# Kernel tuning notes

Hardware: AMD Instinct MI355X
Metric: run time of the kernel (lower is better)

## Reference

```python
import jax, jax.numpy as jnp
import numpy as np

LN_EPS = 1e-12


def setup_inputs() -> dict:
    key = jax.random.key(0)
    ks = jax.random.split(key, 6)
    B, S, H = 32, 512, 768
    P, K = 76, 64
    V, E = 50257, 768
    return {
        "sequence_data": jax.random.normal(ks[0], (B, S, H), dtype=jnp.float32),
        "masked_positions": jax.random.randint(ks[1], (B, P), 0, S, dtype=jnp.int64),
        "candidate_sets": jax.random.randint(ks[2], (B, P, K), 0, V, dtype=jnp.int64),
        "embedding_table": jax.random.normal(ks[3], (V, E), dtype=jnp.float32) * 0.02,
        "dense_w": jax.random.normal(ks[4], (H, E), dtype=jnp.float32) * (1.0 / np.sqrt(H)),
        "dense_b": jnp.zeros((E,), dtype=jnp.float32),
        "ln_gamma": jnp.ones((E,), dtype=jnp.float32),
        "ln_beta": jnp.zeros((E,), dtype=jnp.float32),
    }


def reference(sequence_data, masked_positions, candidate_sets, embedding_table,
              dense_w, dense_b, ln_gamma, ln_beta):
    # Gather masked positions: [B, P, H]
    gathered = jnp.take_along_axis(
        sequence_data, masked_positions[:, :, None], axis=1)
    # Dense (no activation), then LayerNorm (eps=1e-12)
    lm = jnp.einsum('bph,he->bpe', gathered, dense_w) + dense_b
    mu = jnp.mean(lm, axis=-1, keepdims=True)
    var = jnp.mean(jnp.square(lm - mu), axis=-1, keepdims=True)
    lm = (lm - mu) * jax.lax.rsqrt(var + LN_EPS) * ln_gamma + ln_beta
    # Candidate embedding gather: [B, P, K, E]
    cand = embedding_table[candidate_sets]
    # Inner products -> logits [B, P, K]
    logits = jnp.einsum('bpe,bpke->bpk', lm, cand)
    return logits
```

## Files before the change

### kernel.cpp

```cpp
#include <hip/hip_runtime.h>

typedef __attribute__((ext_vector_type(8))) short bf16x8;
typedef __attribute__((ext_vector_type(4))) float f32x4;

#define HH 768
#define EE 768
#define BB 32
#define SS 512
#define PP 76
#define KCAND 64
#define MM (BB * PP)
#define VV 50257
#define NC (MM * KCAND)
#define CAP 16
#define OVF_CAP 4096

#define OFF_WT    0u
#define OFF_AG    1179648u
#define OFF_LM    4915200u
#define OFF_LMN   12386304u
#define OFF_CUR   16121856u
#define OFF_PERM2 16322896u
#define OFF_OVF   19539344u

#define WT_BLOCKS 576
#define AG_BLOCKS 304
#define ZR_BLOCKS 197
#define GEMM_BLOCKS 456
#define SC_BLOCKS 608
#define ROW_BLOCKS 12565
#define OVF_BLOCKS 32

__device__ inline unsigned short f2bf(float f) {
    unsigned int u = __float_as_uint(f);
    u += 0x7fffu + ((u >> 16) & 1u);
    return (unsigned short)(u >> 16);
}
__device__ inline float bf2f(unsigned short h) {
    return __uint_as_float(((unsigned int)h) << 16);
}

__global__ __launch_bounds__(256) void prep_kernel(
    const float* __restrict__ W, unsigned short* __restrict__ Wt,
    const float* __restrict__ seq, const int* __restrict__ mpos,
    unsigned short* __restrict__ Ag, int* __restrict__ cursor) {
    const int bid = blockIdx.x;
    if (bid < WT_BLOCKS) {
        __shared__ float tile[32][33];
        const int h0 = (bid % 24) * 32, e0 = (bid / 24) * 32;
        const int c = threadIdx.x & 31, r = threadIdx.x >> 5;
#pragma unroll
        for (int rr = r; rr < 32; rr += 8)
            tile[rr][c] = W[(size_t)(h0 + rr) * EE + e0 + c];
        __syncthreads();
#pragma unroll
        for (int rr = r; rr < 32; rr += 8)
            Wt[(size_t)(e0 + rr) * HH + h0 + c] = f2bf(tile[c][rr]);
    } else if (bid < WT_BLOCKS + AG_BLOCKS) {
        const int m0 = (bid - WT_BLOCKS) * 8;
        const int t = threadIdx.x;
#pragma unroll
        for (int rr = 0; rr < 8; ++rr) {
            const int m = m0 + rr;
            const int b = m / PP, p = m - b * PP;
            const int ps = mpos[b * PP + p];
            const float* srow = seq + (size_t)(b * SS + ps) * HH;
            unsigned short* drow = Ag + (size_t)m * HH;
#pragma unroll
            for (int j = 0; j < 3; ++j)
                drow[t + j * 256] = f2bf(srow[t + j * 256]);
        }
    } else {
        const int i = (bid - WT_BLOCKS - AG_BLOCKS) * 256 + threadIdx.x;
        if (i <= VV) cursor[i] = 0;
    }
}

__global__ __launch_bounds__(256) void gemm_scatter_kernel(
    const unsigned short* __restrict__ Ag, const unsigned short* __restrict__ Wt,
    float* __restrict__ lm, const int* __restrict__ cand,
    int* __restrict__ cursor, int* __restrict__ perm2, int* __restrict__ ovf) {
    const int bid = blockIdx.x;
    if (bid < GEMM_BLOCKS) {
        __shared__ unsigned short Alds[64][72];
        __shared__ unsigned short Blds[64][72];
        const int bn = bid % 12, bm = bid / 12;
        const int tid = threadIdx.x;
        const int sr = tid >> 2, sc = (tid & 3) * 16;
        const unsigned short* abase = Ag + (size_t)(bm * 64) * HH;
        const unsigned short* bbase = Wt + (size_t)(bn * 64) * HH;
        const int lane = tid & 63, wv = tid >> 6;
        const int wm = wv >> 1, wn = wv & 1;
        const int fr = lane & 15, fq = (lane >> 4) * 8;
        f32x4 acc[2][2] = {};
        for (int kk = 0; kk < HH; kk += 64) {
            __syncthreads();
            *(int4*)&Alds[sr][sc]     = *(const int4*)(abase + (size_t)sr * HH + kk + sc);
            *(int4*)&Alds[sr][sc + 8] = *(const int4*)(abase + (size_t)sr * HH + kk + sc + 8);
            *(int4*)&Blds[sr][sc]     = *(const int4*)(bbase + (size_t)sr * HH + kk + sc);
            *(int4*)&Blds[sr][sc + 8] = *(const int4*)(bbase + (size_t)sr * HH + kk + sc + 8);
            __syncthreads();
#pragma unroll
            for (int ks = 0; ks < 64; ks += 32) {
                bf16x8 af[2], bfr[2];
#pragma unroll
                for (int t = 0; t < 2; ++t)
                    af[t] = *(const bf16x8*)&Alds[wm * 32 + t * 16 + fr][ks + fq];
#pragma unroll
                for (int t = 0; t < 2; ++t)
                    bfr[t] = *(const bf16x8*)&Blds[wn * 32 + t * 16 + fr][ks + fq];
#pragma unroll
                for (int tm = 0; tm < 2; ++tm)
#pragma unroll
                    for (int tn = 0; tn < 2; ++tn)
                        acc[tm][tn] = __builtin_amdgcn_mfma_f32_16x16x32_bf16(
                            af[tm], bfr[tn], acc[tm][tn], 0, 0, 0);
            }
        }
#pragma unroll
        for (int tm = 0; tm < 2; ++tm)
#pragma unroll
            for (int tn = 0; tn < 2; ++tn) {
                const int col = bn * 64 + wn * 32 + tn * 16 + (lane & 15);
                const int rbase = bm * 64 + wm * 32 + tm * 16 + (lane >> 4) * 4;
#pragma unroll
                for (int g = 0; g < 4; ++g)
                    lm[(size_t)(rbase + g) * EE + col] = acc[tm][tn][g];
            }
    } else {
        const int i = (bid - GEMM_BLOCKS) * 256 + threadIdx.x;
        const int row = cand[i];
        const int slot = atomicAdd(&cursor[row], 1);
        if (slot < CAP) {
            perm2[row * CAP + slot] = i;
        } else {
            const int j = atomicAdd(&cursor[VV], 1);
            if (j < OVF_CAP) ovf[j] = i;
        }
    }
}

__global__ __launch_bounds__(256) void ln_kernel(
    const float* __restrict__ lm, const float* __restrict__ bias,
    const float* __restrict__ gamma, const float* __restrict__ beta,
    unsigned short* __restrict__ lmn) {
    const int lane = threadIdx.x & 63;
    const int m = blockIdx.x * 4 + (threadIdx.x >> 6);
    const float4* x4 = (const float4*)(lm + (size_t)m * EE);
    const float4* b4 = (const float4*)bias;
    const float4* g4 = (const float4*)gamma;
    const float4* e4 = (const float4*)beta;
    float x[12], g[12], e[12];
    {
        const float4 X0 = x4[lane * 2], X1 = x4[lane * 2 + 1], X2 = x4[128 + lane];
        const float4 B0 = b4[lane * 2], B1 = b4[lane * 2 + 1], B2 = b4[128 + lane];
        const float4 G0 = g4[lane * 2], G1 = g4[lane * 2 + 1], G2 = g4[128 + lane];
        const float4 E0 = e4[lane * 2], E1 = e4[lane * 2 + 1], E2 = e4[128 + lane];
        x[0]=X0.x+B0.x; x[1]=X0.y+B0.y; x[2]=X0.z+B0.z; x[3]=X0.w+B0.w;
        x[4]=X1.x+B1.x; x[5]=X1.y+B1.y; x[6]=X1.z+B1.z; x[7]=X1.w+B1.w;
        x[8]=X2.x+B2.x; x[9]=X2.y+B2.y; x[10]=X2.z+B2.z; x[11]=X2.w+B2.w;
        g[0]=G0.x; g[1]=G0.y; g[2]=G0.z; g[3]=G0.w;
        g[4]=G1.x; g[5]=G1.y; g[6]=G1.z; g[7]=G1.w;
        g[8]=G2.x; g[9]=G2.y; g[10]=G2.z; g[11]=G2.w;
        e[0]=E0.x; e[1]=E0.y; e[2]=E0.z; e[3]=E0.w;
        e[4]=E1.x; e[5]=E1.y; e[6]=E1.z; e[7]=E1.w;
        e[8]=E2.x; e[9]=E2.y; e[10]=E2.z; e[11]=E2.w;
    }
    float s = 0.f, q = 0.f;
#pragma unroll
    for (int i = 0; i < 12; ++i) { s += x[i]; q += x[i] * x[i]; }
#pragma unroll
    for (int m2 = 32; m2; m2 >>= 1) { s += __shfl_xor(s, m2); q += __shfl_xor(q, m2); }
    const float mu = s * (1.0f / 768.0f);
    const float rstd = rsqrtf(q * (1.0f / 768.0f) - mu * mu + 1e-12f);
    unsigned short o8[8];
#pragma unroll
    for (int i = 0; i < 8; ++i) o8[i] = f2bf((x[i] - mu) * rstd * g[i] + e[i]);
    *(int4*)(lmn + (size_t)m * EE + lane * 8) = *(const int4*)o8;
    unsigned short o4[4];
#pragma unroll
    for (int i = 0; i < 4; ++i) o4[i] = f2bf((x[8 + i] - mu) * rstd * g[8 + i] + e[8 + i]);
    *(ushort2*)(lmn + (size_t)m * EE + 512 + lane * 4) = *(const ushort2*)o4;
    *(ushort2*)(lmn + (size_t)m * EE + 512 + lane * 4 + 2) = *(const ushort2*)(o4 + 2);
}

__global__ __launch_bounds__(256) void group_logits_kernel(
    const float* __restrict__ emb, const unsigned short* __restrict__ lmn,
    const int* __restrict__ cursor, const int* __restrict__ perm2,
    const int* __restrict__ ovf, const int* __restrict__ cand,
    float* __restrict__ out) {
    const int lane = threadIdx.x & 63;
    const int bid = blockIdx.x;
    if (bid < ROW_BLOCKS) {
        const int r = bid * 4 + (threadIdx.x >> 6);
        if (r >= VV) return;
        int c = cursor[r];
        if (c == 0) return;
        if (c > CAP) c = CAP;
        const float4* e4 = (const float4*)(emb + (size_t)r * EE);
        const float4 E0 = e4[lane * 2], E1 = e4[lane * 2 + 1], E2 = e4[128 + lane];
        const int l8 = lane * 8, l4 = 512 + lane * 4;
        const int base = r * CAP;
        for (int o = 0; o < c; o += 4) {
            const int nn = c - o;
            int idxv[4]; bf16x8 c8[4]; ushort4 c4v[4];
#pragma unroll
            for (int j = 0; j < 4; ++j) {
                const int jj = (j < nn) ? j : 0;
                const int idx = perm2[base + o + jj];
                idxv[j] = idx;
                const unsigned short* lrow = lmn + (size_t)(idx >> 6) * EE;
                c8[j] = *(const bf16x8*)(lrow + l8);
                c4v[j] = *(const ushort4*)(lrow + l4);
            }
            float d[4];
#pragma unroll
            for (int j = 0; j < 4; ++j) {
                d[j] = bf2f((unsigned short)c8[j][0]) * E0.x
                     + bf2f((unsigned short)c8[j][1]) * E0.y
                     + bf2f((unsigned short)c8[j][2]) * E0.z
                     + bf2f((unsigned short)c8[j][3]) * E0.w
                     + bf2f((unsigned short)c8[j][4]) * E1.x
                     + bf2f((unsigned short)c8[j][5]) * E1.y
                     + bf2f((unsigned short)c8[j][6]) * E1.z
                     + bf2f((unsigned short)c8[j][7]) * E1.w
                     + bf2f(c4v[j].x) * E2.x + bf2f(c4v[j].y) * E2.y
                     + bf2f(c4v[j].z) * E2.z + bf2f(c4v[j].w) * E2.w;
            }
#pragma unroll
            for (int m2 = 32; m2; m2 >>= 1) {
#pragma unroll
                for (int j = 0; j < 4; ++j) d[j] += __shfl_xor(d[j], m2);
            }
            if (lane == 0) {
#pragma unroll
                for (int j = 0; j < 4; ++j)
                    if (j < nn) out[idxv[j]] = d[j];
            }
        }
    } else {
        const int nov0 = cursor[VV];
        const int nov = nov0 < OVF_CAP ? nov0 : OVF_CAP;
        const int wid = (bid - ROW_BLOCKS) * 4 + (threadIdx.x >> 6);
        const int l8 = lane * 8, l4 = 512 + lane * 4;
        for (int j = wid; j < nov; j += OVF_BLOCKS * 4) {
            const int idx = ovf[j];
            const int r = cand[idx];
            const float4* e4 = (const float4*)(emb + (size_t)r * EE);
            const float4 E0 = e4[lane * 2], E1 = e4[lane * 2 + 1], E2 = e4[128 + lane];
            const unsigned short* lrow = lmn + (size_t)(idx >> 6) * EE;
            const bf16x8 c8 = *(const bf16x8*)(lrow + l8);
            const ushort4 c4v = *(const ushort4*)(lrow + l4);
            float d = bf2f((unsigned short)c8[0]) * E0.x + bf2f((unsigned short)c8[1]) * E0.y
                    + bf2f((unsigned short)c8[2]) * E0.z + bf2f((unsigned short)c8[3]) * E0.w
                    + bf2f((unsigned short)c8[4]) * E1.x + bf2f((unsigned short)c8[5]) * E1.y
                    + bf2f((unsigned short)c8[6]) * E1.z + bf2f((unsigned short)c8[7]) * E1.w
                    + bf2f(c4v.x) * E2.x + bf2f(c4v.y) * E2.y
                    + bf2f(c4v.z) * E2.z + bf2f(c4v.w) * E2.w;
#pragma unroll
            for (int m2 = 32; m2; m2 >>= 1) d += __shfl_xor(d, m2);
            if (lane == 0) out[idx] = d;
        }
    }
}

extern "C" void kernel_launch(void* const* d_in, const int* in_sizes, int n_in,
                              void* d_out, int out_size, void* d_ws, size_t ws_size,
                              hipStream_t stream) {
    const float* seq   = (const float*)d_in[0];
    const int*   mpos  = (const int*)d_in[1];
    const int*   cand  = (const int*)d_in[2];
    const float* emb   = (const float*)d_in[3];
    const float* W     = (const float*)d_in[4];
    const float* bias  = (const float*)d_in[5];
    const float* gamma = (const float*)d_in[6];
    const float* beta  = (const float*)d_in[7];
    float* out = (float*)d_out;

    char* ws = (char*)d_ws;
    unsigned short* Wt   = (unsigned short*)(ws + OFF_WT);
    unsigned short* Ag   = (unsigned short*)(ws + OFF_AG);
    float*          lm   = (float*)(ws + OFF_LM);
    unsigned short* lmn  = (unsigned short*)(ws + OFF_LMN);
    int*            cur  = (int*)(ws + OFF_CUR);
    int*            perm2= (int*)(ws + OFF_PERM2);
    int*            ovf  = (int*)(ws + OFF_OVF);

    prep_kernel<<<WT_BLOCKS + AG_BLOCKS + ZR_BLOCKS, 256, 0, stream>>>(
        W, Wt, seq, mpos, Ag, cur);
    gemm_scatter_kernel<<<GEMM_BLOCKS + SC_BLOCKS, 256, 0, stream>>>(
        Ag, Wt, lm, cand, cur, perm2, ovf);
    ln_kernel<<<MM / 4, 256, 0, stream>>>(lm, bias, gamma, beta, lmn);
    group_logits_kernel<<<ROW_BLOCKS + OVF_BLOCKS, 256, 0, stream>>>(
        emb, lmn, cur, perm2, ovf, cand, out);
}
```

Baseline: 281.1 us.

## Fuse dense GEMM with LayerNorm and move candidate scatter into prep kernel

Replaces the separate GEMM and LayerNorm kernels with one kernel where each block computes 16 full rows of the dense output, reduces row statistics across waves through shared memory, and writes normalized bf16 directly. This removes the fp32 intermediate round trip and one launch. The candidate scatter now runs inside the prep kernel, and cursor zeroing uses a memset. In exchange, every block streams the whole transposed weight matrix through LDS, with only 152 blocks and a sync every 32-wide K step, which may limit GEMM throughput.

```diff
diff --git a/kernel.cpp b/kernel.cpp
--- a/kernel.cpp
+++ b/kernel.cpp
@@ -17,17 +17,15 @@
 
 #define OFF_WT    0u
 #define OFF_AG    1179648u
-#define OFF_LM    4915200u
-#define OFF_LMN   12386304u
-#define OFF_CUR   16121856u
-#define OFF_PERM2 16322896u
-#define OFF_OVF   19539344u
+#define OFF_LMN   4915200u
+#define OFF_CUR   8650752u
+#define OFF_PERM2 8851968u
+#define OFF_OVF   12068416u
 
 #define WT_BLOCKS 576
 #define AG_BLOCKS 304
-#define ZR_BLOCKS 197
-#define GEMM_BLOCKS 456
 #define SC_BLOCKS 608
+#define GLN_BLOCKS 152
 #define ROW_BLOCKS 12565
 #define OVF_BLOCKS 32
 
@@ -40,10 +38,11 @@
     return __uint_as_float(((unsigned int)h) << 16);
 }
 
-__global__ __launch_bounds__(256) void prep_kernel(
+__global__ __launch_bounds__(256) void prep_scatter_kernel(
     const float* __restrict__ W, unsigned short* __restrict__ Wt,
     const float* __restrict__ seq, const int* __restrict__ mpos,
-    unsigned short* __restrict__ Ag, int* __restrict__ cursor) {
+    unsigned short* __restrict__ Ag, const int* __restrict__ cand,
+    int* __restrict__ cursor, int* __restrict__ perm2, int* __restrict__ ovf) {
     const int bid = blockIdx.x;
     if (bid < WT_BLOCKS) {
         __shared__ float tile[32][33];
@@ -72,63 +71,6 @@
         }
     } else {
         const int i = (bid - WT_BLOCKS - AG_BLOCKS) * 256 + threadIdx.x;
-        if (i <= VV) cursor[i] = 0;
-    }
-}
-
-__global__ __launch_bounds__(256) void gemm_scatter_kernel(
-    const unsigned short* __restrict__ Ag, const unsigned short* __restrict__ Wt,
-    float* __restrict__ lm, const int* __restrict__ cand,
-    int* __restrict__ cursor, int* __restrict__ perm2, int* __restrict__ ovf) {
-    const int bid = blockIdx.x;
-    if (bid < GEMM_BLOCKS) {
-        __shared__ unsigned short Alds[64][72];
-        __shared__ unsigned short Blds[64][72];
-        const int bn = bid % 12, bm = bid / 12;
-        const int tid = threadIdx.x;
-        const int sr = tid >> 2, sc = (tid & 3) * 16;
-        const unsigned short* abase = Ag + (size_t)(bm * 64) * HH;
-        const unsigned short* bbase = Wt + (size_t)(bn * 64) * HH;
-        const int lane = tid & 63, wv = tid >> 6;
-        const int wm = wv >> 1, wn = wv & 1;
-        const int fr = lane & 15, fq = (lane >> 4) * 8;
-        f32x4 acc[2][2] = {};
-        for (int kk = 0; kk < HH; kk += 64) {
-            __syncthreads();
-            *(int4*)&Alds[sr][sc]     = *(const int4*)(abase + (size_t)sr * HH + kk + sc);
-            *(int4*)&Alds[sr][sc + 8] = *(const int4*)(abase + (size_t)sr * HH + kk + sc + 8);
-            *(int4*)&Blds[sr][sc]     = *(const int4*)(bbase + (size_t)sr * HH + kk + sc);
-            *(int4*)&Blds[sr][sc + 8] = *(const int4*)(bbase + (size_t)sr * HH + kk + sc + 8);
-            __syncthreads();
-#pragma unroll
-            for (int ks = 0; ks < 64; ks += 32) {
-                bf16x8 af[2], bfr[2];
-#pragma unroll
-                for (int t = 0; t < 2; ++t)
-                    af[t] = *(const bf16x8*)&Alds[wm * 32 + t * 16 + fr][ks + fq];
-#pragma unroll
-                for (int t = 0; t < 2; ++t)
-                    bfr[t] = *(const bf16x8*)&Blds[wn * 32 + t * 16 + fr][ks + fq];
-#pragma unroll
-                for (int tm = 0; tm < 2; ++tm)
-#pragma unroll
-                    for (int tn = 0; tn < 2; ++tn)
-                        acc[tm][tn] = __builtin_amdgcn_mfma_f32_16x16x32_bf16(
-                            af[tm], bfr[tn], acc[tm][tn], 0, 0, 0);
-            }
-        }
-#pragma unroll
-        for (int tm = 0; tm < 2; ++tm)
-#pragma unroll
-            for (int tn = 0; tn < 2; ++tn) {
-                const int col = bn * 64 + wn * 32 + tn * 16 + (lane & 15);
-                const int rbase = bm * 64 + wm * 32 + tm * 16 + (lane >> 4) * 4;
-#pragma unroll
-                for (int g = 0; g < 4; ++g)
-                    lm[(size_t)(rbase + g) * EE + col] = acc[tm][tn][g];
-            }
-    } else {
-        const int i = (bid - GEMM_BLOCKS) * 256 + threadIdx.x;
         const int row = cand[i];
         const int slot = atomicAdd(&cursor[row], 1);
         if (slot < CAP) {
@@ -140,48 +82,86 @@
     }
 }
 
-__global__ __launch_bounds__(256) void ln_kernel(
-    const float* __restrict__ lm, const float* __restrict__ bias,
-    const float* __restrict__ gamma, const float* __restrict__ beta,
-    unsigned short* __restrict__ lmn) {
-    const int lane = threadIdx.x & 63;
-    const int m = blockIdx.x * 4 + (threadIdx.x >> 6);
-    const float4* x4 = (const float4*)(lm + (size_t)m * EE);
-    const float4* b4 = (const float4*)bias;
-    const float4* g4 = (const float4*)gamma;
-    const float4* e4 = (const float4*)beta;
-    float x[12], g[12], e[12];
-    {
-        const float4 X0 = x4[lane * 2], X1 = x4[lane * 2 + 1], X2 = x4[128 + lane];
-        const float4 B0 = b4[lane * 2], B1 = b4[lane * 2 + 1], B2 = b4[128 + lane];
-        const float4 G0 = g4[lane * 2], G1 = g4[lane * 2 + 1], G2 = g4[128 + lane];
-        const float4 E0 = e4[lane * 2], E1 = e4[lane * 2 + 1], E2 = e4[128 + lane];
-        x[0]=X0.x+B0.x; x[1]=X0.y+B0.y; x[2]=X0.z+B0.z; x[3]=X0.w+B0.w;
-        x[4]=X1.x+B1.x; x[5]=X1.y+B1.y; x[6]=X1.z+B1.z; x[7]=X1.w+B1.w;
-        x[8]=X2.x+B2.x; x[9]=X2.y+B2.y; x[10]=X2.z+B2.z; x[11]=X2.w+B2.w;
-        g[0]=G0.x; g[1]=G0.y; g[2]=G0.z; g[3]=G0.w;
-        g[4]=G1.x; g[5]=G1.y; g[6]=G1.z; g[7]=G1.w;
-        g[8]=G2.x; g[9]=G2.y; g[10]=G2.z; g[11]=G2.w;
-        e[0]=E0.x; e[1]=E0.y; e[2]=E0.z; e[3]=E0.w;
-        e[4]=E1.x; e[5]=E1.y; e[6]=E1.z; e[7]=E1.w;
-        e[8]=E2.x; e[9]=E2.y; e[10]=E2.z; e[11]=E2.w;
-    }
-    float s = 0.f, q = 0.f;
-#pragma unroll
-    for (int i = 0; i < 12; ++i) { s += x[i]; q += x[i] * x[i]; }
-#pragma unroll
-    for (int m2 = 32; m2; m2 >>= 1) { s += __shfl_xor(s, m2); q += __shfl_xor(q, m2); }
-    const float mu = s * (1.0f / 768.0f);
-    const float rstd = rsqrtf(q * (1.0f / 768.0f) - mu * mu + 1e-12f);
-    unsigned short o8[8];
-#pragma unroll
-    for (int i = 0; i < 8; ++i) o8[i] = f2bf((x[i] - mu) * rstd * g[i] + e[i]);
-    *(int4*)(lmn + (size_t)m * EE + lane * 8) = *(const int4*)o8;
-    unsigned short o4[4];
-#pragma unroll
-    for (int i = 0; i < 4; ++i) o4[i] = f2bf((x[8 + i] - mu) * rstd * g[8 + i] + e[8 + i]);
-    *(ushort2*)(lmn + (size_t)m * EE + 512 + lane * 4) = *(const ushort2*)o4;
-    *(ushort2*)(lmn + (size_t)m * EE + 512 + lane * 4 + 2) = *(const ushort2*)(o4 + 2);
+__global__ __launch_bounds__(256) void gemm_ln_kernel(
+    const unsigned short* __restrict__ Ag, const unsigned short* __restrict__ Wt,
+    const float* __restrict__ bias, const float* __restrict__ gamma,
+    const float* __restrict__ beta, unsigned short* __restrict__ lmn) {
+    __shared__ unsigned short Blds[768][40];
+    __shared__ unsigned short Alds[16][40];
+    __shared__ float cparam[3 * 768];
+    __shared__ float part[4][16][2];
+    const int tid = threadIdx.x, lane = tid & 63, wv = tid >> 6;
+    const int m0 = blockIdx.x * 16;
+    for (int i = tid; i < 768; i += 256) {
+        cparam[i] = bias[i];
+        cparam[768 + i] = gamma[i];
+        cparam[1536 + i] = beta[i];
+    }
+    const unsigned short* abase = Ag + (size_t)m0 * HH;
+    const int fr = lane & 15, fq = (lane >> 4) * 8;
+    const int sc = (tid & 3) * 8;
+    const int srb = tid >> 2;
+    f32x4 acc[12] = {};
+
+    for (int kk = 0; kk < HH; kk += 32) {
+        __syncthreads();
+#pragma unroll
+        for (int rd = 0; rd < 12; ++rd) {
+            const int n = srb + rd * 64;
+            *(int4*)&Blds[n][sc] = *(const int4*)(Wt + (size_t)n * HH + kk + sc);
+        }
+        if (tid < 64)
+            *(int4*)&Alds[srb][sc] = *(const int4*)(abase + (size_t)srb * HH + kk + sc);
+        __syncthreads();
+        const bf16x8 af = *(const bf16x8*)&Alds[fr][fq];
+#pragma unroll
+        for (int t = 0; t < 12; ++t) {
+            const bf16x8 bf = *(const bf16x8*)&Blds[wv * 192 + t * 16 + fr][fq];
+            acc[t] = __builtin_amdgcn_mfma_f32_16x16x32_bf16(af, bf, acc[t], 0, 0, 0);
+        }
+    }
+    float s[4] = {}, q[4] = {};
+#pragma unroll
+    for (int t = 0; t < 12; ++t) {
+        const int col = wv * 192 + t * 16 + fr;
+        const float b = cparam[col];
+#pragma unroll
+        for (int g = 0; g < 4; ++g) {
+            const float x = acc[t][g] + b;
+            acc[t][g] = x;
+            s[g] += x; q[g] += x * x;
+        }
+    }
+#pragma unroll
+    for (int m2 = 1; m2 < 16; m2 <<= 1) {
+#pragma unroll
+        for (int g = 0; g < 4; ++g) { s[g] += __shfl_xor(s[g], m2); q[g] += __shfl_xor(q[g], m2); }
+    }
+    if (fr == 0) {
+        const int rq = lane >> 4;
+#pragma unroll
+        for (int g = 0; g < 4; ++g) { part[wv][rq * 4 + g][0] = s[g]; part[wv][rq * 4 + g][1] = q[g]; }
+    }
+    __syncthreads();
+    float mu[4], rstd[4];
+#pragma unroll
+    for (int g = 0; g < 4; ++g) {
+        const int r = (lane >> 4) * 4 + g;
+        const float S = part[0][r][0] + part[1][r][0] + part[2][r][0] + part[3][r][0];
+        const float Q = part[0][r][1] + part[1][r][1] + part[2][r][1] + part[3][r][1];
+        mu[g] = S * (1.0f / 768.0f);
+        rstd[g] = rsqrtf(Q * (1.0f / 768.0f) - mu[g] * mu[g] + 1e-12f);
+    }
+#pragma unroll
+    for (int t = 0; t < 12; ++t) {
+        const int col = wv * 192 + t * 16 + fr;
+        const float ga = cparam[768 + col], be = cparam[1536 + col];
+#pragma unroll
+        for (int g = 0; g < 4; ++g) {
+            const int r = m0 + (lane >> 4) * 4 + g;
+            lmn[(size_t)r * EE + col] = f2bf((acc[t][g] - mu[g]) * rstd[g] * ga + be);
+        }
+    }
 }
 
 __global__ __launch_bounds__(256) void group_logits_kernel(
@@ -278,19 +258,17 @@
     float* out = (float*)d_out;
 
     char* ws = (char*)d_ws;
-    unsigned short* Wt   = (unsigned short*)(ws + OFF_WT);
-    unsigned short* Ag   = (unsigned short*)(ws + OFF_AG);
-    float*          lm   = (float*)(ws + OFF_LM);
-    unsigned short* lmn  = (unsigned short*)(ws + OFF_LMN);
-    int*            cur  = (int*)(ws + OFF_CUR);
-    int*            perm2= (int*)(ws + OFF_PERM2);
-    int*            ovf  = (int*)(ws + OFF_OVF);
-
-    prep_kernel<<<WT_BLOCKS + AG_BLOCKS + ZR_BLOCKS, 256, 0, stream>>>(
-        W, Wt, seq, mpos, Ag, cur);
-    gemm_scatter_kernel<<<GEMM_BLOCKS + SC_BLOCKS, 256, 0, stream>>>(
-        Ag, Wt, lm, cand, cur, perm2, ovf);
-    ln_kernel<<<MM / 4, 256, 0, stream>>>(lm, bias, gamma, beta, lmn);
+    unsigned short* Wt    = (unsigned short*)(ws + OFF_WT);
+    unsigned short* Ag    = (unsigned short*)(ws + OFF_AG);
+    unsigned short* lmn   = (unsigned short*)(ws + OFF_LMN);
+    int*            cur   = (int*)(ws + OFF_CUR);
+    int*            perm2 = (int*)(ws + OFF_PERM2);
+    int*            ovf   = (int*)(ws + OFF_OVF);
+
+    hipMemsetAsync(cur, 0, (VV + 1) * sizeof(int), stream);
+    prep_scatter_kernel<<<WT_BLOCKS + AG_BLOCKS + SC_BLOCKS, 256, 0, stream>>>(
+        W, Wt, seq, mpos, Ag, cand, cur, perm2, ovf);
+    gemm_ln_kernel<<<GLN_BLOCKS, 256, 0, stream>>>(Ag, Wt, bias, gamma, beta, lmn);
     group_logits_kernel<<<ROW_BLOCKS + OVF_BLOCKS, 256, 0, stream>>>(
         emb, lmn, cur, perm2, ovf, cand, out);
 }
```

After: 305.7 us. 1.09x slower.
